# Kernel tuning notes

Hardware: AMD Instinct MI355X
Metric: run time of the kernel (lower is better)

Reference implementation:

```python
import jax, jax.numpy as jnp
import numpy as np

N = 100000          # total nodes
E = 3200000         # total edges (avg degree 32)
B = 100             # num graphs
NPG = N // B        # nodes per graph (uniform -> to_dense_batch is a reshape)
D_IN, D_H, D_E, N_CLS = 128, 64, 32, 10


def setup_inputs() -> dict:
    key = jax.random.key(0)
    ks = jax.random.split(key, 12)
    x = jax.random.normal(ks[0], (N, D_IN), jnp.float32)
    # edges strictly within each graph: offset by graph block
    epg = E // B
    offs = (jnp.arange(E, dtype=jnp.int32) // epg) * NPG
    src = jax.random.randint(ks[1], (E,), 0, NPG, jnp.int32) + offs
    dst = jax.random.randint(ks[2], (E,), 0, NPG, jnp.int32) + offs
    edge_index = jnp.stack([src, dst])
    batch = jnp.repeat(jnp.arange(B, dtype=jnp.int32), NPG)

    def glorot(k, fi, fo):
        return jax.random.normal(k, (fi, fo), jnp.float32) * (1.0 / np.sqrt(fi))

    return {
        "x": x, "edge_index": edge_index, "batch": batch,
        "W_a1": glorot(ks[3], D_IN, D_H), "b_a1": jnp.zeros((D_H,), jnp.float32),
        "W_a2": glorot(ks[4], D_H, D_E),  "b_a2": jnp.zeros((D_E,), jnp.float32),
        "W_x1": glorot(ks[5], D_IN, D_H), "b_x1": jnp.zeros((D_H,), jnp.float32),
        "W_x2": glorot(ks[6], D_H, D_E),  "b_x2": jnp.zeros((D_E,), jnp.float32),
        "W_lin": glorot(ks[7], D_E * D_E, N_CLS),
        "b_lin": jnp.zeros((N_CLS,), jnp.float32),
    }


def _gcn(x, W, b, src, dst, n):
    """PyG GCNConv(improved=True): sym-norm with self-loop weight 2."""
    h = x @ W                                                   # [n, out]
    deg = jax.ops.segment_sum(jnp.ones_like(dst, h.dtype), dst, n) + 2.0
    dinv = jax.lax.rsqrt(deg)                                   # [n]
    coef = dinv[src] * dinv[dst]                                # [E]
    agg = jax.ops.segment_sum(h[src] * coef[:, None], dst, n)   # gather-scatter
    agg = agg + (2.0 * dinv * dinv)[:, None] * h                # self-loop term
    return agg + b


def _segment_softmax(v, seg, nseg):
    m = jax.ops.segment_max(v, seg, nseg)
    e = jnp.exp(v - m[seg])
    s = jax.ops.segment_sum(e, seg, nseg)
    return e / s[seg]


def reference(x, edge_index, batch, W_a1, b_a1, W_a2, b_a2,
              W_x1, b_x1, W_x2, b_x2, W_lin, b_lin):
    src, dst = edge_index[0], edge_index[1]
    n = x.shape[0]
    a1 = jax.nn.relu(_gcn(x, W_a1, b_a1, src, dst, n))
    a2 = _segment_softmax(_gcn(a1, W_a2, b_a2, src, dst, n), batch, B)
    x1 = jax.nn.relu(_gcn(x, W_x1, b_x1, src, dst, n))
    x2 = jax.nn.relu(_gcn(x1, W_x2, b_x2, src, dst, n))
    # uniform graph sizes -> to_dense_batch is a reshape (no padding needed)
    a_b = a2.reshape(B, NPG, D_E)
    x_b = x2.reshape(B, NPG, D_E)
    prods = jnp.einsum('bne,bnf->bef', a_b, x_b)   # bmm(a^T, x): [B, D_E, D_E]
    flat = prods.reshape(B, D_E * D_E)
    return jax.nn.softmax(flat @ W_lin + b_lin, axis=-1)
```

## Files before the change

### kernel.cpp

```cpp
#include <hip/hip_runtime.h>
#include <hip/hip_bf16.h>
#include <hip/hip_fp16.h>

#define N_NODES 100000
#define N_EDGES 3200000
#define NB      100
#define NPG     1000
#define EPG     32000
#define DIN     128
#define DH      64
#define DE      32
#define NCLS    10
#define CNT_BLOCKS  832
#define SORT_BLOCKS 416


typedef _Float16 h2_t __attribute__((ext_vector_type(2)));
typedef _Float16 h8_t __attribute__((ext_vector_type(8)));
typedef float    f4_t __attribute__((ext_vector_type(4)));

__device__ __forceinline__ float dot2f(unsigned a, unsigned b, float c) {
#if __has_builtin(__builtin_amdgcn_fdot2)
    return __builtin_amdgcn_fdot2(__builtin_bit_cast(h2_t, a),
                                  __builtin_bit_cast(h2_t, b), c, false);
#else
    float d;
    asm("v_dot2_f32_f16 %0, %1, %2, %3" : "=v"(d) : "v"(a), "v"(b), "v"(c));
    return d;
#endif
}

#define DOT8(rA, rB, dv)                                                        \
    acc[0] = dot2f(__builtin_amdgcn_perm(rB.x, rA.x, 0x05040100u), dv, acc[0]); \
    acc[1] = dot2f(__builtin_amdgcn_perm(rB.x, rA.x, 0x07060302u), dv, acc[1]); \
    acc[2] = dot2f(__builtin_amdgcn_perm(rB.y, rA.y, 0x05040100u), dv, acc[2]); \
    acc[3] = dot2f(__builtin_amdgcn_perm(rB.y, rA.y, 0x07060302u), dv, acc[3]); \
    acc[4] = dot2f(__builtin_amdgcn_perm(rB.z, rA.z, 0x05040100u), dv, acc[4]); \
    acc[5] = dot2f(__builtin_amdgcn_perm(rB.z, rA.z, 0x07060302u), dv, acc[5]); \
    acc[6] = dot2f(__builtin_amdgcn_perm(rB.w, rA.w, 0x05040100u), dv, acc[6]); \
    acc[7] = dot2f(__builtin_amdgcn_perm(rB.w, rA.w, 0x07060302u), dv, acc[7]);


__global__ __launch_bounds__(256) void k_cnt(const int* __restrict__ dst,
                                             int* __restrict__ cnt8) {
    __shared__ int cnt[NPG];
    int slice = blockIdx.x >> 3;
    int g = (blockIdx.x & 7) + 8 * (slice % 13);
    int sub = slice / 13;
    if (g >= NB) return;
    int t = threadIdx.x;
    for (int i = t; i < NPG; i += 256) cnt[i] = 0;
    __syncthreads();
    int ebase = g * EPG + sub * 4000, nbase = g * NPG;
    for (int i = t; i < 4000; i += 256)
        atomicAdd(&cnt[dst[ebase + i] - nbase], 1);
    __syncthreads();
    for (int i = t; i < NPG; i += 256)
        cnt8[sub * N_NODES + nbase + i] = cnt[i];
}


__global__ __launch_bounds__(1024) void k_scan(const int* __restrict__ cnt8,
                                               int* __restrict__ rowptr,
                                               float* __restrict__ dinv,
                                               unsigned short* __restrict__ dh16) {
    __shared__ int sm[1024];
    int g = (blockIdx.x & 7) + 8 * (blockIdx.x >> 3);
    if (g >= NB) return;
    int t = threadIdx.x;
    int nbase = g * NPG, ebase = g * EPG;
    int v = 0;
    if (t < NPG) {
        #pragma unroll
        for (int s8 = 0; s8 < 8; s8++) v += cnt8[s8 * N_NODES + nbase + t];
        float dv = rsqrtf((float)v + 2.0f);
        dinv[nbase + t] = dv;
        dh16[nbase + t] = __half_as_ushort(__float2half_rn(dv));
    }
    sm[t] = v;
    __syncthreads();
    for (int off = 1; off < 1024; off <<= 1) {
        int xx = (t >= off) ? sm[t - off] : 0;
        __syncthreads();
        sm[t] += xx;
        __syncthreads();
    }
    if (t < NPG)
        rowptr[nbase + t] = ebase + sm[t] - v;
    if (g == NB - 1 && t == 0) rowptr[N_NODES] = N_EDGES;
}


union SharedSG {
    struct {
        int cur[256];
        unsigned buf[10000];
    } sc;
    struct {
        __align__(16) unsigned short wt[16384];
    } ge;
};

__global__ __launch_bounds__(1024) void k_sg(const int* __restrict__ src,
                                             const int* __restrict__ dst,
                                             const float* __restrict__ x,
                                             const float* __restrict__ Wa,
                                             const float* __restrict__ Wx,
                                             const int* __restrict__ rowptr,
                                             const unsigned short* __restrict__ dh16,
                                             unsigned int* __restrict__ esrc,
                                             unsigned short* __restrict__ h16) {
    __shared__ SharedSG S;
    int t = threadIdx.x;
    if (blockIdx.x < SORT_BLOCKS) {
        int xcd = blockIdx.x & 7, slot = blockIdx.x >> 3;
        int g = xcd + 8 * (slot % 13);
        int q = slot / 13;
        if (g >= NB) return;
        int nbase = g * NPG, ebase = g * EPG;
        int n0 = q * 250;
        int base0 = rowptr[nbase + n0];
        int cap = rowptr[nbase + n0 + 250] - base0;
        if (t < 250)
            S.sc.cur[t] = rowptr[nbase + n0 + t] - base0;
        __syncthreads();
        for (int i = t; i < EPG; i += 1024) {
            int d = dst[ebase + i] - nbase - n0;
            if ((unsigned)d < 250u) {
                int s = src[ebase + i];
                int pos = atomicAdd(&S.sc.cur[d], 1);
                S.sc.buf[pos] = ((unsigned)(s - nbase) * 16) |
                                ((unsigned)dh16[s] << 16);
            }
        }
        __syncthreads();
        for (int i = t; i < cap; i += 1024)
            esrc[base0 + i] = S.sc.buf[i];
    } else {
        int b2 = blockIdx.x - SORT_BLOCKS;
        int xcd = b2 & 7, slot = b2 >> 3;
        int g = xcd + 8 * (slot >> 2);
        int chunk = slot & 3;
        if (g >= NB) return;
        int row0 = g * NPG + chunk * 250;
        {
            int cc = t & 127, kg = t >> 7;
            const float* Wp = (cc < 64) ? &Wa[cc] : &Wx[cc - 64];
            #pragma unroll
            for (int j = 0; j < 4; j++) {
                int k0 = kg * 16 + j * 4;
                union { __half h[4]; uint2 u; } pk;
                #pragma unroll
                for (int m = 0; m < 4; m++)
                    pk.h[m] = __float2half_rn(Wp[(k0 + m) * 64]);
                int byte = cc * 256 + ((2 * k0) ^ ((cc & 7) << 4));
                *(uint2*)((char*)S.ge.wt + byte) = pk.u;
            }
        }
        __syncthreads();
        int w = t >> 6, l = t & 63;
        int lr = l & 15, kq = l >> 4;
        int rowA = row0 + w * 16 + lr;
        int rA = rowA < N_NODES ? rowA : N_NODES - 1;
        const float* xr = &x[(size_t)rA * 128];
        h8_t a[4];
        #pragma unroll
        for (int kc = 0; kc < 4; kc++) {
            float4 lo = *(const float4*)&xr[kc * 32 + kq * 8];
            float4 hi = *(const float4*)&xr[kc * 32 + kq * 8 + 4];
            h8_t av;
            av[0] = (_Float16)lo.x; av[1] = (_Float16)lo.y;
            av[2] = (_Float16)lo.z; av[3] = (_Float16)lo.w;
            av[4] = (_Float16)hi.x; av[5] = (_Float16)hi.y;
            av[6] = (_Float16)hi.z; av[7] = (_Float16)hi.w;
            a[kc] = av;
        }
        f4_t acc[8] = {};
        #pragma unroll
        for (int kc = 0; kc < 4; kc++) {
            #pragma unroll
            for (int n = 0; n < 8; n++) {
                int cc = n * 16 + lr;
                int byte = cc * 256 + (((kc * 32 + kq * 8) * 2) ^ ((cc & 7) << 4));
                h8_t bf = *(h8_t*)((char*)S.ge.wt + byte);
                acc[n] = __builtin_amdgcn_mfma_f32_16x16x32_f16(a[kc], bf, acc[n], 0, 0, 0);
            }
        }
        int rowD = row0 + w * 16 + kq * 4;
        #pragma unroll
        for (int n = 0; n < 8; n++) {
            #pragma unroll
            for (int j = 0; j < 4; j++) {
                int r = rowD + j;
                if (r < N_NODES)
                    h16[(size_t)r * 128 + n * 16 + lr] =
                        __half_as_ushort(__float2half_rn(acc[n][j]));
            }
        }
    }
}


__global__ __launch_bounds__(256) void k_agg128(const unsigned short* __restrict__ h16,
                                                const int* __restrict__ rowptr,
                                                const unsigned int* __restrict__ esrc,
                                                const float* __restrict__ dinv,
                                                const float* __restrict__ ba,
                                                const float* __restrict__ bx,
                                                unsigned short* __restrict__ outB16) {
    int xcd = blockIdx.x & 7, slot = blockIdx.x >> 3;
    int gi = slot / 250, chunk = slot - gi * 250;
    int g = xcd + 8 * gi;
    if (g >= NB) return;
    int nl   = chunk * 4 + (threadIdx.x >> 6);
    int wid  = g * NPG + nl;
    int lane = threadIdx.x & 63;
    int sub = lane >> 4;
    int cl  = lane & 15;
    const uint4* hg4 = (const uint4*)(h16 + g * NPG * 128);
    float acc[8] = {};
    union U8 { uint4 u; __half h[8]; };
    int e0 = rowptr[wid], e1 = rowptr[wid + 1];
    int e = e0;
    for (; e + 16 <= e1; e += 16) {
        unsigned pv0 = esrc[e + sub];
        unsigned pv1 = esrc[e + 4 + sub];
        unsigned pv2 = esrc[e + 8 + sub];
        unsigned pv3 = esrc[e + 12 + sub];
        uint4 r0 = hg4[(pv0 & 0xffffu) + cl];
        uint4 r1 = hg4[(pv1 & 0xffffu) + cl];
        uint4 r2 = hg4[(pv2 & 0xffffu) + cl];
        uint4 r3 = hg4[(pv3 & 0xffffu) + cl];
        unsigned dA = __builtin_amdgcn_perm(pv1, pv0, 0x07060302u);
        unsigned dB = __builtin_amdgcn_perm(pv3, pv2, 0x07060302u);
        DOT8(r0, r1, dA);
        DOT8(r2, r3, dB);
    }
    for (; e + 8 <= e1; e += 8) {
        unsigned pv0 = esrc[e + sub];
        unsigned pv1 = esrc[e + 4 + sub];
        uint4 r0 = hg4[(pv0 & 0xffffu) + cl];
        uint4 r1 = hg4[(pv1 & 0xffffu) + cl];
        unsigned dA = __builtin_amdgcn_perm(pv1, pv0, 0x07060302u);
        DOT8(r0, r1, dA);
    }
    for (; e < e1; e += 4) {
        int ee = e + sub;
        unsigned pv; float scale;
        if (ee < e1) { pv = esrc[ee]; scale = 1.0f; }
        else         { pv = esrc[e];  scale = 0.0f; }
        U8 r; r.u = hg4[(pv & 0xffffu) + cl];
        float dv = scale * __half2float(__ushort_as_half((unsigned short)(pv >> 16)));
        #pragma unroll
        for (int k = 0; k < 8; k++)
            acc[k] += dv * __half2float(r.h[k]);
    }
    #pragma unroll
    for (int k = 0; k < 8; k++) {
        acc[k] += __shfl_xor(acc[k], 16);
        acc[k] += __shfl_xor(acc[k], 32);
    }
    if (sub == 0) {
        float di = dinv[wid];
        float sw = 2.0f * di * di;
        U8 hv; hv.u = hg4[nl * 16 + cl];
        int cl8 = cl * 8;
        const float* bb = (cl8 < 64) ? &ba[cl8] : &bx[cl8 - 64];
        union { __half2 h[4]; uint4 q; } pk;
        #pragma unroll
        for (int k = 0; k < 4; k++) {
            float ox = fmaxf(di * acc[2 * k]     + sw * __half2float(hv.h[2 * k])     + bb[2 * k],     0.0f);
            float oy = fmaxf(di * acc[2 * k + 1] + sw * __half2float(hv.h[2 * k + 1]) + bb[2 * k + 1], 0.0f);
            pk.h[k] = __floats2half2_rn(ox, oy);
        }
        *(uint4*)&outB16[wid * 128 + cl8] = pk.q;
    }
}


__global__ __launch_bounds__(256) void k_agg64(const unsigned short* __restrict__ g16,
                                               const int* __restrict__ rowptr,
                                               const unsigned int* __restrict__ esrc,
                                               const float* __restrict__ dinv,
                                               const float* __restrict__ ba2,
                                               const float* __restrict__ bx2,
                                               float* __restrict__ s2) {
    int xcd = blockIdx.x & 7, slot = blockIdx.x >> 3;
    int gi = slot / 250, chunk = slot - gi * 250;
    int g = xcd + 8 * gi;
    if (g >= NB) return;
    int nl   = chunk * 4 + (threadIdx.x >> 6);
    int wid  = g * NPG + nl;
    int lane = threadIdx.x & 63;
    int sub = lane >> 3;
    int cl  = lane & 7;
    const uint4* gg4 = (const uint4*)(g16 + g * NPG * 64);
    float acc[8] = {};
    union U8 { uint4 u; __half h[8]; };
    int e0 = rowptr[wid], e1 = rowptr[wid + 1];
    int e = e0;
    for (; e + 16 <= e1; e += 16) {
        unsigned pv0 = esrc[e + sub];
        unsigned pv1 = esrc[e + 8 + sub];
        uint4 r0 = gg4[((pv0 & 0xffffu) >> 1) + cl];
        uint4 r1 = gg4[((pv1 & 0xffffu) >> 1) + cl];
        unsigned dA = __builtin_amdgcn_perm(pv1, pv0, 0x07060302u);
        DOT8(r0, r1, dA);
    }
    for (; e < e1; e += 8) {
        int ee = e + sub;
        unsigned pv; float scale;
        if (ee < e1) { pv = esrc[ee]; scale = 1.0f; }
        else         { pv = esrc[e];  scale = 0.0f; }
        U8 r; r.u = gg4[((pv & 0xffffu) >> 1) + cl];
        float dv = scale * __half2float(__ushort_as_half((unsigned short)(pv >> 16)));
        #pragma unroll
        for (int k = 0; k < 8; k++)
            acc[k] += dv * __half2float(r.h[k]);
    }
    #pragma unroll
    for (int k = 0; k < 8; k++) {
        acc[k] += __shfl_xor(acc[k], 8);
        acc[k] += __shfl_xor(acc[k], 16);
        acc[k] += __shfl_xor(acc[k], 32);
    }
    if (sub == 0) {
        float di = dinv[wid];
        float sw = 2.0f * di * di;
        U8 hv; hv.u = gg4[nl * 8 + cl];
        int cl8 = cl * 8;
        float o[8];
        #pragma unroll
        for (int k = 0; k < 8; k++)
            o[k] = di * acc[k] + sw * __half2float(hv.h[k]);
        if (cl8 < 32) {
            #pragma unroll
            for (int k = 0; k < 8; k++) o[k] += ba2[cl8 + k];
        } else {
            #pragma unroll
            for (int k = 0; k < 8; k++) o[k] = fmaxf(o[k] + bx2[cl8 - 32 + k], 0.0f);
        }
        *(float4*)&s2[wid * 64 + cl8]     = make_float4(o[0], o[1], o[2], o[3]);
        *(float4*)&s2[wid * 64 + cl8 + 4] = make_float4(o[4], o[5], o[6], o[7]);
    }
}


__global__ __launch_bounds__(256) void k_gemm2(const unsigned short* __restrict__ Bm16,
                                               const float* __restrict__ Wa2,
                                               const float* __restrict__ Wx2,
                                               unsigned short* __restrict__ g16) {
    __shared__ float xs[64][132];
    __shared__ float ws[64][68];
    int xcd = blockIdx.x & 7, slot = blockIdx.x >> 3;
    int g = xcd + 8 * (slot >> 4);
    int chunk = slot & 15;
    if (g >= NB) return;
    int row0 = g * NPG + chunk * 64;
    int t = threadIdx.x;
    for (int i = 0; i < 4; i++) {
        int idx = t + 256 * i;
        int k = idx >> 4, c4 = idx & 15, c = c4 * 4;
        float4 v;
        if (c < 32) v = *(const float4*)&Wa2[k * 32 + c];
        else        v = *(const float4*)&Wx2[k * 32 + (c - 32)];
        *(float4*)&ws[k][c] = v;
    }
    for (int i = 0; i < 4; i++) {
        int idx = t + 256 * i;
        int r = idx >> 4, c8 = idx & 15;
        int rr = row0 + r; if (rr >= N_NODES) rr = N_NODES - 1;
        union { uint4 u; __half2 h[4]; } pk;
        pk.u = *(const uint4*)&Bm16[rr * 128 + c8 * 8];
        float2 f0 = __half22float2(pk.h[0]);
        float2 f1 = __half22float2(pk.h[1]);
        float2 f2 = __half22float2(pk.h[2]);
        float2 f3 = __half22float2(pk.h[3]);
        int cb = c8 * 8;
        *(float4*)&xs[r][cb]     = make_float4(f0.x, f0.y, f1.x, f1.y);
        *(float4*)&xs[r][cb + 4] = make_float4(f2.x, f2.y, f3.x, f3.y);
    }
    __syncthreads();
    int cg = t & 15, rg = t >> 4;
    int koff = (cg < 8) ? 0 : 64;
    float acc[4][4] = {};
    for (int k = 0; k < 64; k++) {
        float4 w = *(float4*)&ws[k][cg * 4];
        float xv[4];
        for (int i = 0; i < 4; i++) xv[i] = xs[rg * 4 + i][koff + k];
        for (int i = 0; i < 4; i++) {
            acc[i][0] += xv[i] * w.x; acc[i][1] += xv[i] * w.y;
            acc[i][2] += xv[i] * w.z; acc[i][3] += xv[i] * w.w;
        }
    }
    for (int i = 0; i < 4; i++) {
        int r = row0 + rg * 4 + i;
        if (r < N_NODES) {
            union { ushort4 u; __half2 h[2]; } pk;
            pk.h[0] = __floats2half2_rn(acc[i][0], acc[i][1]);
            pk.h[1] = __floats2half2_rn(acc[i][2], acc[i][3]);
            *(ushort4*)&g16[r * 64 + cg * 4] = pk.u;
        }
    }
}


__global__ __launch_bounds__(512) void k_smax(const float* __restrict__ s2,
                                              float* __restrict__ gmax,
                                              float* __restrict__ sinv) {
    __shared__ float red[16][32];
    int g = (blockIdx.x & 7) + 8 * (blockIdx.x >> 3);
    if (g >= NB) return;
    int t = threadIdx.x;
    int c = t & 31, sub = t >> 5;
    size_t base = (size_t)g * NPG;
    float m = -1e30f;
    for (int n = sub; n < NPG; n += 16)
        m = fmaxf(m, s2[(base + n) * 64 + c]);
    red[sub][c] = m; __syncthreads();
    if (sub == 0) {
        for (int j = 1; j < 16; j++) m = fmaxf(m, red[j][c]);
        red[0][c] = m;
        gmax[g * 32 + c] = m;
    }
    __syncthreads();
    m = red[0][c];
    __syncthreads();
    float sum = 0.0f;
    for (int n = sub; n < NPG; n += 16)
        sum += __expf(s2[(base + n) * 64 + c] - m);
    red[sub][c] = sum; __syncthreads();
    if (sub == 0) {
        for (int j = 1; j < 16; j++) sum += red[j][c];
        sinv[g * 32 + c] = 1.0f / sum;
    }
}


__global__ __launch_bounds__(256) void k_pool(const float* __restrict__ s2,
                                              const float* __restrict__ gmax,
                                              float* __restrict__ prods) {
    __shared__ float ta[25][32];
    __shared__ float tx[25][32];
    __shared__ float gm[32];
    int xcd = blockIdx.x & 7, slot = blockIdx.x >> 3;
    int g = xcd + 8 * (slot >> 3);
    int ch = slot & 7;
    if (g >= NB) return;
    int t = threadIdx.x;
    if (t < 32) gm[t] = gmax[g * 32 + t];
    int e  = t >> 3;
    int f4 = t & 7;
    float a0 = 0.f, a1 = 0.f, a2 = 0.f, a3 = 0.f;
    int base = g * NPG + ch * 125;
    for (int n0 = 0; n0 < 125; n0 += 25) {
        __syncthreads();
        for (int i = t; i < 25 * 16; i += 256) {
            int r = i >> 4, c4 = i & 15;
            float4 v = *(const float4*)&s2[(size_t)(base + n0 + r) * 64 + c4 * 4];
            if (c4 < 8) {
                int cb = c4 * 4;
                v.x = __expf(v.x - gm[cb + 0]);
                v.y = __expf(v.y - gm[cb + 1]);
                v.z = __expf(v.z - gm[cb + 2]);
                v.w = __expf(v.w - gm[cb + 3]);
                *(float4*)&ta[r][cb] = v;
            } else {
                *(float4*)&tx[r][(c4 - 8) * 4] = v;
            }
        }
        __syncthreads();
        #pragma unroll 5
        for (int n = 0; n < 25; n++) {
            float a   = ta[n][e];
            float4 xv = *(float4*)&tx[n][f4 * 4];
            a0 += a * xv.x; a1 += a * xv.y; a2 += a * xv.z; a3 += a * xv.w;
        }
    }
    *(float4*)&prods[((size_t)(g * 8 + ch)) * 1024 + e * 32 + f4 * 4] =
        make_float4(a0, a1, a2, a3);
}


__global__ __launch_bounds__(256) void k_head(const float* __restrict__ prods,
                                              const float* __restrict__ sinv,
                                              const float* __restrict__ Wlin,
                                              const float* __restrict__ blin,
                                              float* __restrict__ out) {
    __shared__ float red[4][NCLS];
    int g = (blockIdx.x & 7) + 8 * (blockIdx.x >> 3);
    if (g >= NB) return;
    int t = threadIdx.x;
    float p[NCLS];
    for (int c = 0; c < NCLS; c++) p[c] = 0.0f;
    const float* pg = &prods[(size_t)g * 8 * 1024];
    for (int j = 0; j < 4; j++) {
        int k = t * 4 + j;
        int e = k >> 5;
        float v = 0.0f;
        #pragma unroll
        for (int q = 0; q < 8; q++) v += pg[q * 1024 + k];
        v *= sinv[g * 32 + e];
        const float* wrow = &Wlin[k * NCLS];
        for (int c = 0; c < NCLS; c++) p[c] += v * wrow[c];
    }
    for (int off = 32; off > 0; off >>= 1)
        for (int c = 0; c < NCLS; c++) p[c] += __shfl_down(p[c], off, 64);
    int wave = t >> 6, lane = t & 63;
    if (lane == 0)
        for (int c = 0; c < NCLS; c++) red[wave][c] = p[c];
    __syncthreads();
    if (t == 0) {
        float logits[NCLS]; float mx = -1e30f;
        for (int c = 0; c < NCLS; c++) {
            logits[c] = red[0][c] + red[1][c] + red[2][c] + red[3][c] + blin[c];
            mx = fmaxf(mx, logits[c]);
        }
        float s = 0.0f;
        for (int c = 0; c < NCLS; c++) { logits[c] = expf(logits[c] - mx); s += logits[c]; }
        float inv = 1.0f / s;
        for (int c = 0; c < NCLS; c++) out[g * NCLS + c] = logits[c] * inv;
    }
}


extern "C" void kernel_launch(void* const* d_in, const int* in_sizes, int n_in,
                              void* d_out, int out_size, void* d_ws, size_t ws_size,
                              hipStream_t stream) {
    const float* x    = (const float*)d_in[0];
    const int*   ei   = (const int*)d_in[1];
    const float* Wa1  = (const float*)d_in[3];
    const float* ba1  = (const float*)d_in[4];
    const float* Wa2  = (const float*)d_in[5];
    const float* ba2  = (const float*)d_in[6];
    const float* Wx1  = (const float*)d_in[7];
    const float* bx1  = (const float*)d_in[8];
    const float* Wx2  = (const float*)d_in[9];
    const float* bx2  = (const float*)d_in[10];
    const float* Wlin = (const float*)d_in[11];
    const float* blin = (const float*)d_in[12];
    float* out = (float*)d_out;

    char* w = (char*)d_ws;
    auto alloc = [&](size_t bytes) -> void* {
        void* p = (void*)w;
        w += (bytes + 255) & ~(size_t)255;
        return p;
    };
    int*            rowptr = (int*)alloc((N_NODES + 1) * sizeof(int));
    int*            cnt8   = (int*)alloc((size_t)8 * N_NODES * sizeof(int));
    float*          dinv   = (float*)alloc(N_NODES * sizeof(float));
    unsigned short* dh16   = (unsigned short*)alloc(N_NODES * sizeof(unsigned short));
    unsigned int*   esrc   = (unsigned int*)alloc((size_t)N_EDGES * sizeof(unsigned int));
    float*          gmax   = (float*)alloc(NB * DE * sizeof(float));
    float*          sinv   = (float*)alloc(NB * DE * sizeof(float));
    float*          prods  = (float*)alloc((size_t)NB * 8 * 1024 * sizeof(float));
    unsigned short* h16    = (unsigned short*)alloc((size_t)N_NODES * 128 * sizeof(unsigned short));
    unsigned short* b16    = (unsigned short*)alloc((size_t)N_NODES * 128 * sizeof(unsigned short));
    unsigned short* g16    = (unsigned short*)alloc((size_t)N_NODES * 64 * sizeof(unsigned short));
    float*          s2     = (float*)alloc((size_t)N_NODES * 64 * sizeof(float));

    const int* srcp = ei;
    const int* dstp = ei + N_EDGES;

    k_cnt<<<CNT_BLOCKS, 256, 0, stream>>>(dstp, cnt8);
    k_scan<<<8 * 13, 1024, 0, stream>>>(cnt8, rowptr, dinv, dh16);
    k_sg<<<SORT_BLOCKS + 8 * 13 * 4, 1024, 0, stream>>>(srcp, dstp, x, Wa1, Wx1,
                                                        rowptr, dh16, esrc, h16);
    k_agg128<<<8 * 13 * 250, 256, 0, stream>>>(h16, rowptr, esrc, dinv, ba1, bx1, b16);
    k_gemm2<<<8 * 13 * 16, 256, 0, stream>>>(b16, Wa2, Wx2, g16);
    k_agg64<<<8 * 13 * 250, 256, 0, stream>>>(g16, rowptr, esrc, dinv, ba2, bx2, s2);
    k_smax<<<8 * 13, 512, 0, stream>>>(s2, gmax, sinv);
    k_pool<<<8 * 13 * 8, 256, 0, stream>>>(s2, gmax, prods);
    k_head<<<8 * 13, 256, 0, stream>>>(prods, sinv, Wlin, blin, out);
}
```

Measured before the change: 326.5 us.

## Map one node per lane group in aggregation kernels, dropping cross-lane reductions

The two gather-aggregate kernels previously gave each node a whole wavefront, with sub-groups splitting the edges and a shuffle reduction at the end. Now each node gets a 16-lane (128-wide) or 8-lane (64-wide) group that walks all its edges serially, with 8-way unrolled gathers, a paired tail and an odd-edge tail. This removes the shuffle reductions, the idle lanes in the epilogue and most of the launched blocks. In exchange each group has a longer serial edge loop and some lanes are wasted on clamped out-of-range nodes. Some index arithmetic is also widened to size_t.

Result: faster. 303.0 us (-7.2%).

```diff
diff --git a/kernel.cpp b/kernel.cpp
--- a/kernel.cpp
+++ b/kernel.cpp
@@ -209,72 +209,70 @@
                                                 const float* __restrict__ bx,
                                                 unsigned short* __restrict__ outB16) {
     int xcd = blockIdx.x & 7, slot = blockIdx.x >> 3;
-    int gi = slot / 250, chunk = slot - gi * 250;
+    int gi = slot / 63, chunk = slot - gi * 63;
     int g = xcd + 8 * gi;
     if (g >= NB) return;
-    int nl   = chunk * 4 + (threadIdx.x >> 6);
-    int wid  = g * NPG + nl;
-    int lane = threadIdx.x & 63;
-    int sub = lane >> 4;
-    int cl  = lane & 15;
+    int grp = threadIdx.x >> 4;
+    int cl  = threadIdx.x & 15;
+    int nl  = chunk * 16 + grp;
+    int valid = nl < NPG;
+    int nlc = valid ? nl : NPG - 1;
+    int wid = g * NPG + nlc;
     const uint4* hg4 = (const uint4*)(h16 + g * NPG * 128);
     float acc[8] = {};
     union U8 { uint4 u; __half h[8]; };
-    int e0 = rowptr[wid], e1 = rowptr[wid + 1];
+    int e0 = rowptr[wid];
+    int e1 = valid ? rowptr[wid + 1] : e0;
     int e = e0;
-    for (; e + 16 <= e1; e += 16) {
-        unsigned pv0 = esrc[e + sub];
-        unsigned pv1 = esrc[e + 4 + sub];
-        unsigned pv2 = esrc[e + 8 + sub];
-        unsigned pv3 = esrc[e + 12 + sub];
+    for (; e + 8 <= e1; e += 8) {
+        unsigned pv0 = esrc[e + 0], pv1 = esrc[e + 1];
+        unsigned pv2 = esrc[e + 2], pv3 = esrc[e + 3];
+        unsigned pv4 = esrc[e + 4], pv5 = esrc[e + 5];
+        unsigned pv6 = esrc[e + 6], pv7 = esrc[e + 7];
         uint4 r0 = hg4[(pv0 & 0xffffu) + cl];
         uint4 r1 = hg4[(pv1 & 0xffffu) + cl];
         uint4 r2 = hg4[(pv2 & 0xffffu) + cl];
         uint4 r3 = hg4[(pv3 & 0xffffu) + cl];
+        uint4 r4 = hg4[(pv4 & 0xffffu) + cl];
+        uint4 r5 = hg4[(pv5 & 0xffffu) + cl];
+        uint4 r6 = hg4[(pv6 & 0xffffu) + cl];
+        uint4 r7 = hg4[(pv7 & 0xffffu) + cl];
         unsigned dA = __builtin_amdgcn_perm(pv1, pv0, 0x07060302u);
         unsigned dB = __builtin_amdgcn_perm(pv3, pv2, 0x07060302u);
+        unsigned dC = __builtin_amdgcn_perm(pv5, pv4, 0x07060302u);
+        unsigned dD = __builtin_amdgcn_perm(pv7, pv6, 0x07060302u);
         DOT8(r0, r1, dA);
         DOT8(r2, r3, dB);
-    }
-    for (; e + 8 <= e1; e += 8) {
-        unsigned pv0 = esrc[e + sub];
-        unsigned pv1 = esrc[e + 4 + sub];
+        DOT8(r4, r5, dC);
+        DOT8(r6, r7, dD);
+    }
+    for (; e + 2 <= e1; e += 2) {
+        unsigned pv0 = esrc[e], pv1 = esrc[e + 1];
         uint4 r0 = hg4[(pv0 & 0xffffu) + cl];
         uint4 r1 = hg4[(pv1 & 0xffffu) + cl];
         unsigned dA = __builtin_amdgcn_perm(pv1, pv0, 0x07060302u);
         DOT8(r0, r1, dA);
     }
-    for (; e < e1; e += 4) {
-        int ee = e + sub;
-        unsigned pv; float scale;
-        if (ee < e1) { pv = esrc[ee]; scale = 1.0f; }
-        else         { pv = esrc[e];  scale = 0.0f; }
-        U8 r; r.u = hg4[(pv & 0xffffu) + cl];
-        float dv = scale * __half2float(__ushort_as_half((unsigned short)(pv >> 16)));
-        #pragma unroll
-        for (int k = 0; k < 8; k++)
-            acc[k] += dv * __half2float(r.h[k]);
-    }
+    if (e < e1) {
+        unsigned pv = esrc[e];
+        uint4 r = hg4[(pv & 0xffffu) + cl];
+        unsigned dA = pv >> 16;
+        DOT8(r, r, dA);
+    }
+    float di = dinv[wid];
+    float sw = 2.0f * di * di;
+    U8 hv; hv.u = hg4[nlc * 16 + cl];
+    int cl8 = cl * 8;
+    const float* bb = (cl8 < 64) ? &ba[cl8] : &bx[cl8 - 64];
+    union { __half2 h[4]; uint4 q; } pk;
     #pragma unroll
-    for (int k = 0; k < 8; k++) {
-        acc[k] += __shfl_xor(acc[k], 16);
-        acc[k] += __shfl_xor(acc[k], 32);
-    }
-    if (sub == 0) {
-        float di = dinv[wid];
-        float sw = 2.0f * di * di;
-        U8 hv; hv.u = hg4[nl * 16 + cl];
-        int cl8 = cl * 8;
-        const float* bb = (cl8 < 64) ? &ba[cl8] : &bx[cl8 - 64];
-        union { __half2 h[4]; uint4 q; } pk;
-        #pragma unroll
-        for (int k = 0; k < 4; k++) {
-            float ox = fmaxf(di * acc[2 * k]     + sw * __half2float(hv.h[2 * k])     + bb[2 * k],     0.0f);
-            float oy = fmaxf(di * acc[2 * k + 1] + sw * __half2float(hv.h[2 * k + 1]) + bb[2 * k + 1], 0.0f);
-            pk.h[k] = __floats2half2_rn(ox, oy);
-        }
-        *(uint4*)&outB16[wid * 128 + cl8] = pk.q;
-    }
+    for (int k = 0; k < 4; k++) {
+        float ox = fmaxf(di * acc[2 * k]     + sw * __half2float(hv.h[2 * k])     + bb[2 * k],     0.0f);
+        float oy = fmaxf(di * acc[2 * k + 1] + sw * __half2float(hv.h[2 * k + 1]) + bb[2 * k + 1], 0.0f);
+        pk.h[k] = __floats2half2_rn(ox, oy);
+    }
+    if (valid)
+        *(uint4*)&outB16[(size_t)wid * 128 + cl8] = pk.q;
 }
 
 
@@ -286,62 +284,74 @@
                                                const float* __restrict__ bx2,
                                                float* __restrict__ s2) {
     int xcd = blockIdx.x & 7, slot = blockIdx.x >> 3;
-    int gi = slot / 250, chunk = slot - gi * 250;
+    int gi = slot >> 5, chunk = slot & 31;
     int g = xcd + 8 * gi;
     if (g >= NB) return;
-    int nl   = chunk * 4 + (threadIdx.x >> 6);
-    int wid  = g * NPG + nl;
-    int lane = threadIdx.x & 63;
-    int sub = lane >> 3;
-    int cl  = lane & 7;
+    int grp = threadIdx.x >> 3;
+    int cl  = threadIdx.x & 7;
+    int nl  = chunk * 32 + grp;
+    int valid = nl < NPG;
+    int nlc = valid ? nl : NPG - 1;
+    int wid = g * NPG + nlc;
     const uint4* gg4 = (const uint4*)(g16 + g * NPG * 64);
     float acc[8] = {};
     union U8 { uint4 u; __half h[8]; };
-    int e0 = rowptr[wid], e1 = rowptr[wid + 1];
+    int e0 = rowptr[wid];
+    int e1 = valid ? rowptr[wid + 1] : e0;
     int e = e0;
-    for (; e + 16 <= e1; e += 16) {
-        unsigned pv0 = esrc[e + sub];
-        unsigned pv1 = esrc[e + 8 + sub];
+    for (; e + 8 <= e1; e += 8) {
+        unsigned pv0 = esrc[e + 0], pv1 = esrc[e + 1];
+        unsigned pv2 = esrc[e + 2], pv3 = esrc[e + 3];
+        unsigned pv4 = esrc[e + 4], pv5 = esrc[e + 5];
+        unsigned pv6 = esrc[e + 6], pv7 = esrc[e + 7];
+        uint4 r0 = gg4[((pv0 & 0xffffu) >> 1) + cl];
+        uint4 r1 = gg4[((pv1 & 0xffffu) >> 1) + cl];
+        uint4 r2 = gg4[((pv2 & 0xffffu) >> 1) + cl];
+        uint4 r3 = gg4[((pv3 & 0xffffu) >> 1) + cl];
+        uint4 r4 = gg4[((pv4 & 0xffffu) >> 1) + cl];
+        uint4 r5 = gg4[((pv5 & 0xffffu) >> 1) + cl];
+        uint4 r6 = gg4[((pv6 & 0xffffu) >> 1) + cl];
+        uint4 r7 = gg4[((pv7 & 0xffffu) >> 1) + cl];
+        unsigned dA = __builtin_amdgcn_perm(pv1, pv0, 0x07060302u);
+        unsigned dB = __builtin_amdgcn_perm(pv3, pv2, 0x07060302u);
+        unsigned dC = __builtin_amdgcn_perm(pv5, pv4, 0x07060302u);
+        unsigned dD = __builtin_amdgcn_perm(pv7, pv6, 0x07060302u);
+        DOT8(r0, r1, dA);
+        DOT8(r2, r3, dB);
+        DOT8(r4, r5, dC);
+        DOT8(r6, r7, dD);
+    }
+    for (; e + 2 <= e1; e += 2) {
+        unsigned pv0 = esrc[e], pv1 = esrc[e + 1];
         uint4 r0 = gg4[((pv0 & 0xffffu) >> 1) + cl];
         uint4 r1 = gg4[((pv1 & 0xffffu) >> 1) + cl];
         unsigned dA = __builtin_amdgcn_perm(pv1, pv0, 0x07060302u);
         DOT8(r0, r1, dA);
     }
-    for (; e < e1; e += 8) {
-        int ee = e + sub;
-        unsigned pv; float scale;
-        if (ee < e1) { pv = esrc[ee]; scale = 1.0f; }
-        else         { pv = esrc[e];  scale = 0.0f; }
-        U8 r; r.u = gg4[((pv & 0xffffu) >> 1) + cl];
-        float dv = scale * __half2float(__ushort_as_half((unsigned short)(pv >> 16)));
-        #pragma unroll
-        for (int k = 0; k < 8; k++)
-            acc[k] += dv * __half2float(r.h[k]);
-    }
+    if (e < e1) {
+        unsigned pv = esrc[e];
+        uint4 r = gg4[((pv & 0xffffu) >> 1) + cl];
+        unsigned dA = pv >> 16;
+        DOT8(r, r, dA);
+    }
+    float di = dinv[wid];
+    float sw = 2.0f * di * di;
+    U8 hv; hv.u = gg4[nlc * 8 + cl];
+    int cl8 = cl * 8;
+    float o[8];
     #pragma unroll
-    for (int k = 0; k < 8; k++) {
-        acc[k] += __shfl_xor(acc[k], 8);
-        acc[k] += __shfl_xor(acc[k], 16);
-        acc[k] += __shfl_xor(acc[k], 32);
-    }
-    if (sub == 0) {
-        float di = dinv[wid];
-        float sw = 2.0f * di * di;
-        U8 hv; hv.u = gg4[nl * 8 + cl];
-        int cl8 = cl * 8;
-        float o[8];
-        #pragma unroll
-        for (int k = 0; k < 8; k++)
-            o[k] = di * acc[k] + sw * __half2float(hv.h[k]);
-        if (cl8 < 32) {
-            #pragma unroll
-            for (int k = 0; k < 8; k++) o[k] += ba2[cl8 + k];
-        } else {
-            #pragma unroll
-            for (int k = 0; k < 8; k++) o[k] = fmaxf(o[k] + bx2[cl8 - 32 + k], 0.0f);
-        }
-        *(float4*)&s2[wid * 64 + cl8]     = make_float4(o[0], o[1], o[2], o[3]);
-        *(float4*)&s2[wid * 64 + cl8 + 4] = make_float4(o[4], o[5], o[6], o[7]);
+    for (int k = 0; k < 8; k++)
+        o[k] = di * acc[k] + sw * __half2float(hv.h[k]);
+    if (cl8 < 32) {
+        #pragma unroll
+        for (int k = 0; k < 8; k++) o[k] += ba2[cl8 + k];
+    } else {
+        #pragma unroll
+        for (int k = 0; k < 8; k++) o[k] = fmaxf(o[k] + bx2[cl8 - 32 + k], 0.0f);
+    }
+    if (valid) {
+        *(float4*)&s2[(size_t)wid * 64 + cl8]     = make_float4(o[0], o[1], o[2], o[3]);
+        *(float4*)&s2[(size_t)wid * 64 + cl8 + 4] = make_float4(o[4], o[5], o[6], o[7]);
     }
 }
 
@@ -371,7 +381,7 @@
         int r = idx >> 4, c8 = idx & 15;
         int rr = row0 + r; if (rr >= N_NODES) rr = N_NODES - 1;
         union { uint4 u; __half2 h[4]; } pk;
-        pk.u = *(const uint4*)&Bm16[rr * 128 + c8 * 8];
+        pk.u = *(const uint4*)&Bm16[(size_t)rr * 128 + c8 * 8];
         float2 f0 = __half22float2(pk.h[0]);
         float2 f1 = __half22float2(pk.h[1]);
         float2 f2 = __half22float2(pk.h[2]);
@@ -399,7 +409,7 @@
             union { ushort4 u; __half2 h[2]; } pk;
             pk.h[0] = __floats2half2_rn(acc[i][0], acc[i][1]);
             pk.h[1] = __floats2half2_rn(acc[i][2], acc[i][3]);
-            *(ushort4*)&g16[r * 64 + cg * 4] = pk.u;
+            *(ushort4*)&g16[(size_t)r * 64 + cg * 4] = pk.u;
         }
     }
 }
@@ -567,9 +577,9 @@
     k_scan<<<8 * 13, 1024, 0, stream>>>(cnt8, rowptr, dinv, dh16);
     k_sg<<<SORT_BLOCKS + 8 * 13 * 4, 1024, 0, stream>>>(srcp, dstp, x, Wa1, Wx1,
                                                         rowptr, dh16, esrc, h16);
-    k_agg128<<<8 * 13 * 250, 256, 0, stream>>>(h16, rowptr, esrc, dinv, ba1, bx1, b16);
+    k_agg128<<<8 * 13 * 63, 256, 0, stream>>>(h16, rowptr, esrc, dinv, ba1, bx1, b16);
     k_gemm2<<<8 * 13 * 16, 256, 0, stream>>>(b16, Wa2, Wx2, g16);
-    k_agg64<<<8 * 13 * 250, 256, 0, stream>>>(g16, rowptr, esrc, dinv, ba2, bx2, s2);
+    k_agg64<<<8 * 13 * 32, 256, 0, stream>>>(g16, rowptr, esrc, dinv, ba2, bx2, s2);
     k_smax<<<8 * 13, 512, 0, stream>>>(s2, gmax, sinv);
     k_pool<<<8 * 13 * 8, 256, 0, stream>>>(s2, gmax, prods);
     k_head<<<8 * 13, 256, 0, stream>>>(prods, sinv, Wlin, blin, out);
```
